# Optimization experiments

Hardware: AMD Instinct MI355X
Metric: run time of the kernel (lower is better)

Reference implementation:

```python
import jax, jax.numpy as jnp
import numpy as np

LN_EPS = 1e-5


def setup_inputs() -> dict:
    key = jax.random.key(0)
    k1, k2, k3 = jax.random.split(key, 3)
    B, L, D = 8, 2048, 512
    K, Dc = 8192, 16
    x = jax.random.normal(k1, (B, L, D), dtype=jnp.float32)
    # xavier_uniform for Linear(dim -> codebook_dim), weight shape (Dc, D)
    bound = float(np.sqrt(6.0 / (D + Dc)))
    proj_weight = jax.random.uniform(k2, (Dc, D), dtype=jnp.float32, minval=-bound, maxval=bound)
    codebook = jax.random.normal(k3, (K, Dc), dtype=jnp.float32)
    return {"x": x, "proj_weight": proj_weight, "codebook": codebook}


def reference(x, proj_weight, codebook):
    # random projection: (B,L,D) @ (D,Dc) -> (B,L,Dc)
    h = jnp.einsum("bld,cd->blc", x, proj_weight)
    # LayerNorm over last dim, no affine params
    mu = jnp.mean(h, axis=-1, keepdims=True)
    var = jnp.mean(jnp.square(h - mu), axis=-1, keepdims=True)
    h = (h - mu) / jnp.sqrt(var + LN_EPS)
    # squared-distance via dot-product decomposition; avoids (B,L,K,Dc) blowup.
    # argmin of ||h - c||^2 == argmin of ||h - c|| (sqrt is monotone).
    h2 = jnp.sum(jnp.square(h), axis=-1, keepdims=True)        # (B,L,1)
    c2 = jnp.sum(jnp.square(codebook), axis=-1)                # (K,)
    dots = jnp.einsum("blc,kc->blk", h, codebook)              # (B,L,K)
    dist2 = h2 - 2.0 * dots + c2                               # (B,L,K)
    codes = jnp.argmin(dist2, axis=-1)                         # (B,L) int
    return codes
```

## Files before the change

kernel.cpp:

```cpp
#include <hip/hip_runtime.h>
#include <math.h>

#define LN_EPS 1e-5f

typedef _Float16 f16;
typedef _Float16 f16x8 __attribute__((ext_vector_type(8)));
typedef float f32x4 __attribute__((ext_vector_type(4)));

constexpr int DC = 16;
constexpr int K = 8192;
constexpr int NTOK = 16384;
constexpr int D = 512;
constexpr float SCALE = 16384.f;
constexpr float EPS_S = LN_EPS * SCALE * SCALE;

__global__ __launch_bounds__(256) void prep_cb(const float* __restrict__ cb,
                                               f16* __restrict__ cbA,
                                               float* __restrict__ c2s) {
  const int tid = threadIdx.x;
  const int ti = tid >> 6;
  const int l = tid & 63;
  const int ct = blockIdx.x * 4 + ti;
  const int code = ct * 16 + (l & 15);
  const int g = l >> 4;

  const float* row = cb + (size_t)code * DC + (g & 1) * 8;
  f32x4 v0 = *(const f32x4*)row;
  f32x4 v1 = *(const f32x4*)(row + 4);
  float vv[8] = {v0[0], v0[1], v0[2], v0[3], v1[0], v1[1], v1[2], v1[3]};

  f16x8 r;
#pragma unroll
  for (int p = 0; p < 8; ++p) {
    float cc = -128.f * vv[p];
    f16 hh = (f16)cc;
    r[p] = (g < 2) ? hh : (f16)(cc - (float)hh);
  }
  *(f16x8*)(cbA + ((size_t)ct * 64 + l) * 8) = r;

  if (g == 0) {
    const f32x4* rw = (const f32x4*)(cb + (size_t)code * DC);
    f32x4 a0 = rw[0], a1 = rw[1], a2 = rw[2], a3 = rw[3];
    float s = 0.f;
#pragma unroll
    for (int p = 0; p < 4; ++p)
      s += a0[p] * a0[p] + a1[p] * a1[p] + a2[p] * a2[p] + a3[p] * a3[p];
    c2s[code] = (s + 16.5f) * SCALE;
  }
}

__global__ __launch_bounds__(1024, 4) void fused(
    const float* __restrict__ x, const float* __restrict__ wq,
    const float* __restrict__ cb, const f16* __restrict__ cbA,
    const float* __restrict__ c2s, int* __restrict__ out) {
  __shared__ float comb[16 * 320];
  __shared__ float hsm[64][17];
  __shared__ float fin_d[16][64];
  __shared__ int fin_t[16][64];

  const int tid = threadIdx.x;
  const int w = tid >> 6;
  const int lane = tid & 63;
  const int g = lane >> 4;
  const int col = lane & 15;
  const int doff = (g & 1) * 8;
  const int tb = blockIdx.x * 64;

  const int j = w & 3;
  const int dq = w >> 2;

  f16x8 aw[8];
#pragma unroll
  for (int st = 0; st < 8; ++st) {
    const int step = dq * 8 + st;
    const float* wp = wq + (size_t)col * D + step * 16 + doff;
    f32x4 u0 = *(const f32x4*)wp;
    f32x4 u1 = *(const f32x4*)(wp + 4);
    float v[8] = {u0[0], u0[1], u0[2], u0[3], u1[0], u1[1], u1[2], u1[3]};
    f16x8 r;
#pragma unroll
    for (int p = 0; p < 8; ++p) {
      float f = v[p] * 64.f;
      f16 h1 = (f16)f;
      r[p] = (g < 2) ? h1 : (f16)(f - (float)h1);
    }
    aw[st] = r;
  }

  f32x4 acc = {0.f, 0.f, 0.f, 0.f};
  const float* xrow = x + (size_t)(tb + j * 16 + col) * D;
#pragma unroll
  for (int st = 0; st < 8; ++st) {
    const int step = dq * 8 + st;
    const float* xp = xrow + step * 16 + doff;
    f32x4 u0 = *(const f32x4*)xp;
    f32x4 u1 = *(const f32x4*)(xp + 4);
    float v[8] = {u0[0], u0[1], u0[2], u0[3], u1[0], u1[1], u1[2], u1[3]};
    f16x8 bh, bl;
#pragma unroll
    for (int p = 0; p < 8; ++p) {
      float f = v[p] * 256.f;
      f16 h1 = (f16)f;
      bh[p] = h1;
      bl[p] = (f16)(f - (float)h1);
    }
    f16x8 b1 = (g < 2) ? bh : bl;
    f16x8 b2 = (g < 2) ? bl : bh;
    acc = __builtin_amdgcn_mfma_f32_16x16x32_f16(aw[st], b1, acc, 0, 0, 0);
    acc = __builtin_amdgcn_mfma_f32_16x16x32_f16(aw[st], b2, acc, 0, 0, 0);
  }
  *(f32x4*)&comb[w * 320 + col * 20 + g * 4] = acc;
  __syncthreads();

  const int tokL = tid >> 4;
  const int cL = tid & 15;
  const int jL = tokL >> 4;
  const int colL = tokL & 15;
  float hv = (comb[(0 * 4 + jL) * 320 + colL * 20 + cL] +
              comb[(1 * 4 + jL) * 320 + colL * 20 + cL]) +
             (comb[(2 * 4 + jL) * 320 + colL * 20 + cL] +
              comb[(3 * 4 + jL) * 320 + colL * 20 + cL]);
  float s = hv;
  s += __shfl_xor(s, 1, 16);
  s += __shfl_xor(s, 2, 16);
  s += __shfl_xor(s, 4, 16);
  s += __shfl_xor(s, 8, 16);
  float mu = s * (1.f / 16.f);
  float diff = hv - mu;
  float v2 = diff * diff;
  v2 += __shfl_xor(v2, 1, 16);
  v2 += __shfl_xor(v2, 2, 16);
  v2 += __shfl_xor(v2, 4, 16);
  v2 += __shfl_xor(v2, 8, 16);
  float var = v2 * (1.f / 16.f);
  hsm[tokL][cL] = diff / sqrtf(var + EPS_S);
  __syncthreads();

  f16x8 b1[4], b2[4];
#pragma unroll
  for (int jj = 0; jj < 4; ++jj) {
#pragma unroll
    for (int p = 0; p < 8; ++p) {
      float f = hsm[jj * 16 + col][doff + p] * 256.f;
      f16 h1 = (f16)f;
      f16 l1 = (f16)(f - (float)h1);
      b1[jj][p] = (g < 2) ? h1 : l1;
      b2[jj][p] = (g < 2) ? l1 : h1;
    }
  }

  const int q = w;
  float best[4] = {3.0e38f, 3.0e38f, 3.0e38f, 3.0e38f};
  int btg[4] = {0, 0, 0, 0};

#pragma unroll 4
  for (int t = 0; t < 32; ++t) {
    const int ktile = q * 32 + t;
    f16x8 a = *(const f16x8*)&cbA[((size_t)ktile * 64 + lane) * 8];
    f32x4 c2v = *(const f32x4*)&c2s[ktile * 16 + g * 4];
    const int tag = t * 4 + g;
#pragma unroll
    for (int jj = 0; jj < 4; ++jj) {
      f32x4 ac = __builtin_amdgcn_mfma_f32_16x16x32_f16(a, b1[jj], c2v, 0, 0, 0);
      ac = __builtin_amdgcn_mfma_f32_16x16x32_f16(a, b2[jj], ac, 0, 0, 0);
      float m = fminf(fminf(ac[0], ac[1]), fminf(ac[2], ac[3]));
      bool lt = m < best[jj];
      best[jj] = lt ? m : best[jj];
      btg[jj] = lt ? tag : btg[jj];
    }
  }

#pragma unroll
  for (int jj = 0; jj < 4; ++jj) {
    float d = best[jj];
    int tg = btg[jj];
#pragma unroll
    for (int off = 16; off <= 32; off <<= 1) {
      float od = __shfl_xor(d, off);
      int otg = __shfl_xor(tg, off);
      bool take = (od < d) || (od == d && otg < tg);
      d = take ? od : d;
      tg = take ? otg : tg;
    }
    if (lane < 16) {
      fin_d[q][jj * 16 + lane] = d;
      fin_t[q][jj * 16 + lane] = tg;
    }
  }
  __syncthreads();

  if (tid < 64) {
    const int tok = tid;
    float bd = fin_d[0][tok];
    int btag = fin_t[0][tok];
    int bq = 0;
#pragma unroll
    for (int q2 = 1; q2 < 16; ++q2) {
      float d2 = fin_d[q2][tok];
      int t2 = fin_t[q2][tok];
      bool take = (d2 < bd) || (d2 == bd && false);
      bd = take ? d2 : bd;
      btag = take ? t2 : btag;
      bq = take ? q2 : bq;
    }
    const int k0 = bq * 512 + (btag >> 2) * 16 + (btag & 3) * 4;

    float h[16];
#pragma unroll
    for (int dd = 0; dd < 16; ++dd) h[dd] = hsm[tok][dd];

    float bestd = 3.0e38f;
    int bestk = k0;
#pragma unroll
    for (int r = 0; r < 4; ++r) {
      const int kk = k0 + r;
      const float* crow = cb + (size_t)kk * DC;
      float sd = 0.f;
#pragma unroll
      for (int dd = 0; dd < 16; ++dd) {
        float df = h[dd] - crow[dd];
        sd = fmaf(df, df, sd);
      }
      if (sd < bestd) {
        bestd = sd;
        bestk = kk;
      }
    }
    out[tb + tok] = bestk;
  }
}

extern "C" void kernel_launch(void* const* d_in, const int* in_sizes, int n_in,
                              void* d_out, int out_size, void* d_ws,
                              size_t ws_size, hipStream_t stream) {
  const float* x = (const float*)d_in[0];
  const float* w = (const float*)d_in[1];
  const float* cb = (const float*)d_in[2];

  f16* cbA = (f16*)d_ws;
  float* c2s = (float*)(cbA + (size_t)K * 32);

  prep_cb<<<K / 64, 256, 0, stream>>>(cb, cbA, c2s);
  fused<<<NTOK / 64, 1024, 0, stream>>>(x, w, cb, cbA, c2s, (int*)d_out);
}
```

Baseline: 45.36 us.

## Shrink token tiles, precompute weight split, and refine argmin over code groups

The fused kernel now processes 32 tokens per 512-thread block, with 8 waves each scanning 1024 codes. The projection weights are split into hi/lo fp16 once in the prep kernel instead of in every block. The inner argmin loop tracks only a running min per group of 8 tiles, with no per-tile tag, and then rescans 32 candidate codes in fp32 across 16 lanes per token. Hi/lo splitting uses a bitmask plus packed conversion, and x loads are hoisted ahead of the MFMAs. The trade-off is more blocks, a larger exact-rescan stage per token, and a small extra prep block.

After: 40.43 us. 10.9% less time.

```diff
diff --git a/kernel.cpp b/kernel.cpp
--- a/kernel.cpp
+++ b/kernel.cpp
@@ -5,6 +5,8 @@
 
 typedef _Float16 f16;
 typedef _Float16 f16x8 __attribute__((ext_vector_type(8)));
+typedef _Float16 f16x2 __attribute__((ext_vector_type(2)));
+typedef __fp16 fp16x2 __attribute__((ext_vector_type(2)));
 typedef float f32x4 __attribute__((ext_vector_type(4)));
 
 constexpr int DC = 16;
@@ -14,10 +16,59 @@
 constexpr float SCALE = 16384.f;
 constexpr float EPS_S = LN_EPS * SCALE * SCALE;
 
-__global__ __launch_bounds__(256) void prep_cb(const float* __restrict__ cb,
-                                               f16* __restrict__ cbA,
-                                               float* __restrict__ c2s) {
+static __device__ __forceinline__ f16x8 mk8(f16x2 a, f16x2 b, f16x2 c,
+                                            f16x2 d) {
+  union {
+    f16x2 p[4];
+    f16x8 v;
+  } u;
+  u.p[0] = a;
+  u.p[1] = b;
+  u.p[2] = c;
+  u.p[3] = d;
+  return u.v;
+}
+
+static __device__ __forceinline__ void hilo2(float f0, float f1, f16x2& ph,
+                                             f16x2& pl) {
+  float h0 = __uint_as_float(__float_as_uint(f0) & 0xFFFFE000u);
+  float h1 = __uint_as_float(__float_as_uint(f1) & 0xFFFFE000u);
+  ph = __builtin_bit_cast(f16x2, __builtin_amdgcn_cvt_pkrtz(h0, h1));
+  pl = __builtin_bit_cast(f16x2,
+                          __builtin_amdgcn_cvt_pkrtz(f0 - h0, f1 - h1));
+}
+
+__global__ __launch_bounds__(256) void prep(const float* __restrict__ cb,
+                                            const float* __restrict__ wq,
+                                            f16* __restrict__ cbA,
+                                            float* __restrict__ c2s,
+                                            f16* __restrict__ wAf) {
   const int tid = threadIdx.x;
+
+  if (blockIdx.x == K / 64) {
+#pragma unroll
+    for (int i = 0; i < 8; ++i) {
+      int slot = tid + 256 * i;
+      int tile = slot >> 6;
+      int l = slot & 63;
+      int g = l >> 4;
+      int col = l & 15;
+      int doff = (g & 1) * 8;
+      const float* wp = wq + (size_t)col * D + tile * 16 + doff;
+      f32x4 u0 = *(const f32x4*)wp;
+      f32x4 u1 = *(const f32x4*)(wp + 4);
+      f16x2 ph[4], pl[4];
+      hilo2(u0[0] * 64.f, u0[1] * 64.f, ph[0], pl[0]);
+      hilo2(u0[2] * 64.f, u0[3] * 64.f, ph[1], pl[1]);
+      hilo2(u1[0] * 64.f, u1[1] * 64.f, ph[2], pl[2]);
+      hilo2(u1[2] * 64.f, u1[3] * 64.f, ph[3], pl[3]);
+      f16x8 hi = mk8(ph[0], ph[1], ph[2], ph[3]);
+      f16x8 lo = mk8(pl[0], pl[1], pl[2], pl[3]);
+      *(f16x8*)(wAf + (size_t)slot * 8) = (g < 2) ? hi : lo;
+    }
+    return;
+  }
+
   const int ti = tid >> 6;
   const int l = tid & 63;
   const int ct = blockIdx.x * 4 + ti;
@@ -27,16 +78,14 @@
   const float* row = cb + (size_t)code * DC + (g & 1) * 8;
   f32x4 v0 = *(const f32x4*)row;
   f32x4 v1 = *(const f32x4*)(row + 4);
-  float vv[8] = {v0[0], v0[1], v0[2], v0[3], v1[0], v1[1], v1[2], v1[3]};
-
-  f16x8 r;
-#pragma unroll
-  for (int p = 0; p < 8; ++p) {
-    float cc = -128.f * vv[p];
-    f16 hh = (f16)cc;
-    r[p] = (g < 2) ? hh : (f16)(cc - (float)hh);
-  }
-  *(f16x8*)(cbA + ((size_t)ct * 64 + l) * 8) = r;
+  f16x2 ph[4], pl[4];
+  hilo2(v0[0] * -128.f, v0[1] * -128.f, ph[0], pl[0]);
+  hilo2(v0[2] * -128.f, v0[3] * -128.f, ph[1], pl[1]);
+  hilo2(v1[0] * -128.f, v1[1] * -128.f, ph[2], pl[2]);
+  hilo2(v1[2] * -128.f, v1[3] * -128.f, ph[3], pl[3]);
+  f16x8 hi = mk8(ph[0], ph[1], ph[2], ph[3]);
+  f16x8 lo = mk8(pl[0], pl[1], pl[2], pl[3]);
+  *(f16x8*)(cbA + ((size_t)ct * 64 + l) * 8) = (g < 2) ? hi : lo;
 
   if (g == 0) {
     const f32x4* rw = (const f32x4*)(cb + (size_t)code * DC);
@@ -49,14 +98,14 @@
   }
 }
 
-__global__ __launch_bounds__(1024, 4) void fused(
-    const float* __restrict__ x, const float* __restrict__ wq,
-    const float* __restrict__ cb, const f16* __restrict__ cbA,
-    const float* __restrict__ c2s, int* __restrict__ out) {
-  __shared__ float comb[16 * 320];
-  __shared__ float hsm[64][17];
-  __shared__ float fin_d[16][64];
-  __shared__ int fin_t[16][64];
+__global__ __launch_bounds__(512, 4) void fused(
+    const float* __restrict__ x, const float* __restrict__ cb,
+    const f16* __restrict__ cbA, const float* __restrict__ c2s,
+    const f16* __restrict__ wAf, int* __restrict__ out) {
+  __shared__ float comb[8 * 16 * 20];
+  __shared__ float hsm[32 * 20];
+  __shared__ float fin_d[8][32];
+  __shared__ int fin_t[8][32];
 
   const int tid = threadIdx.x;
   const int w = tid >> 6;
@@ -64,62 +113,49 @@
   const int g = lane >> 4;
   const int col = lane & 15;
   const int doff = (g & 1) * 8;
-  const int tb = blockIdx.x * 64;
-
-  const int j = w & 3;
-  const int dq = w >> 2;
-
+  const int tb = blockIdx.x * 32;
+
+  const int j = w & 1;
+  const int dq = w >> 1;
+
+  const float* xrow = x + (size_t)(tb + j * 16 + col) * D + dq * 128 + doff;
+  f32x4 xu0[8], xu1[8];
+#pragma unroll
+  for (int st = 0; st < 8; ++st) {
+    xu0[st] = *(const f32x4*)(xrow + st * 16);
+    xu1[st] = *(const f32x4*)(xrow + st * 16 + 4);
+  }
   f16x8 aw[8];
 #pragma unroll
+  for (int st = 0; st < 8; ++st)
+    aw[st] = *(const f16x8*)(wAf + ((size_t)(dq * 8 + st) * 64 + lane) * 8);
+
+  f32x4 acc = {0.f, 0.f, 0.f, 0.f};
+#pragma unroll
   for (int st = 0; st < 8; ++st) {
-    const int step = dq * 8 + st;
-    const float* wp = wq + (size_t)col * D + step * 16 + doff;
-    f32x4 u0 = *(const f32x4*)wp;
-    f32x4 u1 = *(const f32x4*)(wp + 4);
-    float v[8] = {u0[0], u0[1], u0[2], u0[3], u1[0], u1[1], u1[2], u1[3]};
-    f16x8 r;
-#pragma unroll
-    for (int p = 0; p < 8; ++p) {
-      float f = v[p] * 64.f;
-      f16 h1 = (f16)f;
-      r[p] = (g < 2) ? h1 : (f16)(f - (float)h1);
-    }
-    aw[st] = r;
-  }
-
-  f32x4 acc = {0.f, 0.f, 0.f, 0.f};
-  const float* xrow = x + (size_t)(tb + j * 16 + col) * D;
-#pragma unroll
-  for (int st = 0; st < 8; ++st) {
-    const int step = dq * 8 + st;
-    const float* xp = xrow + step * 16 + doff;
-    f32x4 u0 = *(const f32x4*)xp;
-    f32x4 u1 = *(const f32x4*)(xp + 4);
-    float v[8] = {u0[0], u0[1], u0[2], u0[3], u1[0], u1[1], u1[2], u1[3]};
-    f16x8 bh, bl;
-#pragma unroll
-    for (int p = 0; p < 8; ++p) {
-      float f = v[p] * 256.f;
-      f16 h1 = (f16)f;
-      bh[p] = h1;
-      bl[p] = (f16)(f - (float)h1);
-    }
+    f16x2 ph[4], pl[4];
+    hilo2(xu0[st][0] * 256.f, xu0[st][1] * 256.f, ph[0], pl[0]);
+    hilo2(xu0[st][2] * 256.f, xu0[st][3] * 256.f, ph[1], pl[1]);
+    hilo2(xu1[st][0] * 256.f, xu1[st][1] * 256.f, ph[2], pl[2]);
+    hilo2(xu1[st][2] * 256.f, xu1[st][3] * 256.f, ph[3], pl[3]);
+    f16x8 bh = mk8(ph[0], ph[1], ph[2], ph[3]);
+    f16x8 bl = mk8(pl[0], pl[1], pl[2], pl[3]);
     f16x8 b1 = (g < 2) ? bh : bl;
     f16x8 b2 = (g < 2) ? bl : bh;
     acc = __builtin_amdgcn_mfma_f32_16x16x32_f16(aw[st], b1, acc, 0, 0, 0);
     acc = __builtin_amdgcn_mfma_f32_16x16x32_f16(aw[st], b2, acc, 0, 0, 0);
   }
-  *(f32x4*)&comb[w * 320 + col * 20 + g * 4] = acc;
+  *(f32x4*)&comb[(w * 16 + col) * 20 + g * 4] = acc;
   __syncthreads();
 
   const int tokL = tid >> 4;
   const int cL = tid & 15;
   const int jL = tokL >> 4;
   const int colL = tokL & 15;
-  float hv = (comb[(0 * 4 + jL) * 320 + colL * 20 + cL] +
-              comb[(1 * 4 + jL) * 320 + colL * 20 + cL]) +
-             (comb[(2 * 4 + jL) * 320 + colL * 20 + cL] +
-              comb[(3 * 4 + jL) * 320 + colL * 20 + cL]);
+  float hv = (comb[((0 * 2 + jL) * 16 + colL) * 20 + cL] +
+              comb[((1 * 2 + jL) * 16 + colL) * 20 + cL]) +
+             (comb[((2 * 2 + jL) * 16 + colL) * 20 + cL] +
+              comb[((3 * 2 + jL) * 16 + colL) * 20 + cL]);
   float s = hv;
   s += __shfl_xor(s, 1, 16);
   s += __shfl_xor(s, 2, 16);
@@ -133,101 +169,126 @@
   v2 += __shfl_xor(v2, 4, 16);
   v2 += __shfl_xor(v2, 8, 16);
   float var = v2 * (1.f / 16.f);
-  hsm[tokL][cL] = diff / sqrtf(var + EPS_S);
+  hsm[tokL * 20 + cL] = diff / sqrtf(var + EPS_S);
   __syncthreads();
 
-  f16x8 b1[4], b2[4];
-#pragma unroll
-  for (int jj = 0; jj < 4; ++jj) {
-#pragma unroll
-    for (int p = 0; p < 8; ++p) {
-      float f = hsm[jj * 16 + col][doff + p] * 256.f;
-      f16 h1 = (f16)f;
-      f16 l1 = (f16)(f - (float)h1);
-      b1[jj][p] = (g < 2) ? h1 : l1;
-      b2[jj][p] = (g < 2) ? l1 : h1;
+  f16x8 b1[2], b2[2];
+#pragma unroll
+  for (int jj = 0; jj < 2; ++jj) {
+    const float* hp = &hsm[(jj * 16 + col) * 20 + doff];
+    f32x4 u0 = *(const f32x4*)hp;
+    f32x4 u1 = *(const f32x4*)(hp + 4);
+    f16x2 ph[4], pl[4];
+    hilo2(u0[0] * 256.f, u0[1] * 256.f, ph[0], pl[0]);
+    hilo2(u0[2] * 256.f, u0[3] * 256.f, ph[1], pl[1]);
+    hilo2(u1[0] * 256.f, u1[1] * 256.f, ph[2], pl[2]);
+    hilo2(u1[2] * 256.f, u1[3] * 256.f, ph[3], pl[3]);
+    f16x8 bh = mk8(ph[0], ph[1], ph[2], ph[3]);
+    f16x8 bl = mk8(pl[0], pl[1], pl[2], pl[3]);
+    b1[jj] = (g < 2) ? bh : bl;
+    b2[jj] = (g < 2) ? bl : bh;
+  }
+
+  const int q = w;
+  float best0 = 3.0e38f, best1 = 3.0e38f;
+  int grp0 = 0, grp1 = 0;
+  const f16* pa = cbA + ((size_t)q * 64 * 64 + lane) * 8;
+  const float* pc = c2s + q * 1024 + g * 4;
+
+  for (int gi = 0; gi < 8; ++gi) {
+    float sb0 = best0, sb1 = best1;
+#pragma unroll
+    for (int ti = 0; ti < 8; ++ti) {
+      int t = gi * 8 + ti;
+      f16x8 a = *(const f16x8*)(pa + (size_t)t * 512);
+      f32x4 c2v = *(const f32x4*)(pc + t * 16);
+      f32x4 a0 = __builtin_amdgcn_mfma_f32_16x16x32_f16(a, b1[0], c2v, 0, 0, 0);
+      a0 = __builtin_amdgcn_mfma_f32_16x16x32_f16(a, b2[0], a0, 0, 0, 0);
+      f32x4 a1 = __builtin_amdgcn_mfma_f32_16x16x32_f16(a, b1[1], c2v, 0, 0, 0);
+      a1 = __builtin_amdgcn_mfma_f32_16x16x32_f16(a, b2[1], a1, 0, 0, 0);
+      best0 = fminf(best0, fminf(fminf(a0[0], a0[1]), fminf(a0[2], a0[3])));
+      best1 = fminf(best1, fminf(fminf(a1[0], a1[1]), fminf(a1[2], a1[3])));
     }
-  }
-
-  const int q = w;
-  float best[4] = {3.0e38f, 3.0e38f, 3.0e38f, 3.0e38f};
-  int btg[4] = {0, 0, 0, 0};
-
-#pragma unroll 4
-  for (int t = 0; t < 32; ++t) {
-    const int ktile = q * 32 + t;
-    f16x8 a = *(const f16x8*)&cbA[((size_t)ktile * 64 + lane) * 8];
-    f32x4 c2v = *(const f32x4*)&c2s[ktile * 16 + g * 4];
-    const int tag = t * 4 + g;
-#pragma unroll
-    for (int jj = 0; jj < 4; ++jj) {
-      f32x4 ac = __builtin_amdgcn_mfma_f32_16x16x32_f16(a, b1[jj], c2v, 0, 0, 0);
-      ac = __builtin_amdgcn_mfma_f32_16x16x32_f16(a, b2[jj], ac, 0, 0, 0);
-      float m = fminf(fminf(ac[0], ac[1]), fminf(ac[2], ac[3]));
-      bool lt = m < best[jj];
-      best[jj] = lt ? m : best[jj];
-      btg[jj] = lt ? tag : btg[jj];
+    grp0 = (best0 < sb0) ? gi : grp0;
+    grp1 = (best1 < sb1) ? gi : grp1;
+  }
+
+  int tg0 = grp0 * 4 + g, tg1 = grp1 * 4 + g;
+#pragma unroll
+  for (int off = 16; off <= 32; off <<= 1) {
+    float od = __shfl_xor(best0, off);
+    int ot = __shfl_xor(tg0, off);
+    bool tk = (od < best0) || (od == best0 && ot < tg0);
+    best0 = tk ? od : best0;
+    tg0 = tk ? ot : tg0;
+    od = __shfl_xor(best1, off);
+    ot = __shfl_xor(tg1, off);
+    tk = (od < best1) || (od == best1 && ot < tg1);
+    best1 = tk ? od : best1;
+    tg1 = tk ? ot : tg1;
+  }
+  if (lane < 16) {
+    fin_d[q][lane] = best0;
+    fin_t[q][lane] = tg0;
+    fin_d[q][16 + lane] = best1;
+    fin_t[q][16 + lane] = tg1;
+  }
+  __syncthreads();
+
+  const int tok = tid >> 4;
+  const int c = tid & 15;
+  float bd = fin_d[0][tok];
+  int btag = fin_t[0][tok];
+  int bq = 0;
+#pragma unroll
+  for (int q2 = 1; q2 < 8; ++q2) {
+    float d2 = fin_d[q2][tok];
+    int t2 = fin_t[q2][tok];
+    bool tk = d2 < bd;
+    bd = tk ? d2 : bd;
+    btag = tk ? t2 : btag;
+    bq = tk ? q2 : bq;
+  }
+  const int kb = bq * 1024 + (btag >> 2) * 128 + (btag & 3) * 4;
+
+  f32x4 h0 = *(const f32x4*)&hsm[tok * 20];
+  f32x4 h1 = *(const f32x4*)&hsm[tok * 20 + 4];
+  f32x4 h2 = *(const f32x4*)&hsm[tok * 20 + 8];
+  f32x4 h3 = *(const f32x4*)&hsm[tok * 20 + 12];
+
+  float bestd = 3.0e38f;
+  int bestk = kb;
+#pragma unroll
+  for (int e2 = 0; e2 < 2; ++e2) {
+    int e = c * 2 + e2;
+    int kk = kb + (e >> 2) * 16 + (e & 3);
+    const f32x4* cr = (const f32x4*)(cb + (size_t)kk * DC);
+    f32x4 c0 = cr[0], c1 = cr[1], c2r = cr[2], c3 = cr[3];
+    float sd = 0.f;
+#pragma unroll
+    for (int p = 0; p < 4; ++p) {
+      float d0 = h0[p] - c0[p];
+      float d1 = h1[p] - c1[p];
+      float dd2 = h2[p] - c2r[p];
+      float d3 = h3[p] - c3[p];
+      sd = fmaf(d0, d0, sd);
+      sd = fmaf(d1, d1, sd);
+      sd = fmaf(dd2, dd2, sd);
+      sd = fmaf(d3, d3, sd);
     }
-  }
-
-#pragma unroll
-  for (int jj = 0; jj < 4; ++jj) {
-    float d = best[jj];
-    int tg = btg[jj];
-#pragma unroll
-    for (int off = 16; off <= 32; off <<= 1) {
-      float od = __shfl_xor(d, off);
-      int otg = __shfl_xor(tg, off);
-      bool take = (od < d) || (od == d && otg < tg);
-      d = take ? od : d;
-      tg = take ? otg : tg;
-    }
-    if (lane < 16) {
-      fin_d[q][jj * 16 + lane] = d;
-      fin_t[q][jj * 16 + lane] = tg;
-    }
-  }
-  __syncthreads();
-
-  if (tid < 64) {
-    const int tok = tid;
-    float bd = fin_d[0][tok];
-    int btag = fin_t[0][tok];
-    int bq = 0;
-#pragma unroll
-    for (int q2 = 1; q2 < 16; ++q2) {
-      float d2 = fin_d[q2][tok];
-      int t2 = fin_t[q2][tok];
-      bool take = (d2 < bd) || (d2 == bd && false);
-      bd = take ? d2 : bd;
-      btag = take ? t2 : btag;
-      bq = take ? q2 : bq;
-    }
-    const int k0 = bq * 512 + (btag >> 2) * 16 + (btag & 3) * 4;
-
-    float h[16];
-#pragma unroll
-    for (int dd = 0; dd < 16; ++dd) h[dd] = hsm[tok][dd];
-
-    float bestd = 3.0e38f;
-    int bestk = k0;
-#pragma unroll
-    for (int r = 0; r < 4; ++r) {
-      const int kk = k0 + r;
-      const float* crow = cb + (size_t)kk * DC;
-      float sd = 0.f;
-#pragma unroll
-      for (int dd = 0; dd < 16; ++dd) {
-        float df = h[dd] - crow[dd];
-        sd = fmaf(df, df, sd);
-      }
-      if (sd < bestd) {
-        bestd = sd;
-        bestk = kk;
-      }
-    }
-    out[tb + tok] = bestk;
-  }
+    bool tk = sd < bestd;
+    bestd = tk ? sd : bestd;
+    bestk = tk ? kk : bestk;
+  }
+#pragma unroll
+  for (int off = 1; off < 16; off <<= 1) {
+    float od = __shfl_xor(bestd, off, 16);
+    int ok = __shfl_xor(bestk, off, 16);
+    bool tk = (od < bestd) || (od == bestd && ok < bestk);
+    bestd = tk ? od : bestd;
+    bestk = tk ? ok : bestk;
+  }
+  if (c == 0) out[tb + tok] = bestk;
 }
 
 extern "C" void kernel_launch(void* const* d_in, const int* in_sizes, int n_in,
@@ -239,7 +300,8 @@
 
   f16* cbA = (f16*)d_ws;
   float* c2s = (float*)(cbA + (size_t)K * 32);
-
-  prep_cb<<<K / 64, 256, 0, stream>>>(cb, cbA, c2s);
-  fused<<<NTOK / 64, 1024, 0, stream>>>(x, w, cb, cbA, c2s, (int*)d_out);
-}
+  f16* wAf = (f16*)(c2s + K);
+
+  prep<<<K / 64 + 1, 256, 0, stream>>>(cb, w, cbA, c2s, wAf);
+  fused<<<NTOK / 32, 512, 0, stream>>>(x, cb, cbA, c2s, wAf, (int*)d_out);
+}
```
